# Performance work log

Hardware: AMD Instinct MI355X
Metric: run time of the kernel (lower is better)

## Reference

```python
import jax, jax.numpy as jnp
import numpy as np

K = 3          # kernel size
PAD = 1        # (K-1)//2, stride=1, dilation=1


def _modulated_deform_conv(depth, offset, mask, w, b):
    """torchvision deform_conv2d with in_ch=out_ch=1, stride=1, pad=1, dil=1.
    depth:  [B,1,H,W]
    offset: [B,2*K*K,H,W]  interleaved (dy, dx) per kernel tap
    mask:   [B,K*K,H,W]    modulation scalars
    w:      [1,1,K,K]      conv weights (ones buffer)
    b:      [1]            bias (zeros buffer)
    """
    B, _, H, W = depth.shape
    kk = K * K
    img = depth[:, 0]                                    # [B,H,W]

    off = offset.reshape(B, kk, 2, H, W)
    dy, dx = off[:, :, 0], off[:, :, 1]                  # [B,kk,H,W]

    # integer tap offsets of the 3x3 kernel
    ky, kx = jnp.meshgrid(jnp.arange(K), jnp.arange(K), indexing='ij')
    ky = ky.reshape(kk).astype(depth.dtype)
    kx = kx.reshape(kk).astype(depth.dtype)

    iy = jnp.arange(H, dtype=depth.dtype)
    ix = jnp.arange(W, dtype=depth.dtype)
    # sampling coords per output pixel per tap: [B,kk,H,W]
    y = iy[None, None, :, None] - PAD + ky[None, :, None, None] + dy
    x = ix[None, None, None, :] - PAD + kx[None, :, None, None] + dx

    y0f = jnp.floor(y); x0f = jnp.floor(x)
    wy = y - y0f; wx = x - x0f                           # frac parts
    y0 = y0f.astype(jnp.int32); x0 = x0f.astype(jnp.int32)
    y1 = y0 + 1;  x1 = x0 + 1

    bidx = jnp.arange(B)[:, None, None, None]

    def corner(yc, xc):
        inb = (yc >= 0) & (yc < H) & (xc >= 0) & (xc < W)
        v = img[bidx, jnp.clip(yc, 0, H - 1), jnp.clip(xc, 0, W - 1)]
        return jnp.where(inb, v, jnp.zeros((), depth.dtype))

    sampled = (corner(y0, x0) * (1 - wy) * (1 - wx)
             + corner(y0, x1) * (1 - wy) * wx
             + corner(y1, x0) * wy * (1 - wx)
             + corner(y1, x1) * wy * wx)                 # [B,kk,H,W]

    wk = w.reshape(1, kk, 1, 1)
    out = jnp.sum(sampled * mask * wk, axis=1) + b[0]    # [B,H,W]
    return out[:, None]                                  # [B,1,H,W]


def setup_inputs() -> dict:
    key = jax.random.key(0)
    k1, k2, k3 = jax.random.split(key, 3)
    B, H, W = 8, 512, 512
    depth  = jax.random.normal(k1, (B, 1, H, W), dtype=jnp.float32)
    weight = jax.random.uniform(k2, (B, K * K, H, W), dtype=jnp.float32)
    offset = jax.random.normal(k3, (B, 2 * K * K, H, W), dtype=jnp.float32)
    w = jnp.ones((1, 1, K, K), dtype=jnp.float32)   # buffer 'w'
    b = jnp.zeros((1,), dtype=jnp.float32)          # buffer 'b'
    return {"depth": depth, "weight": weight, "offset": offset, "w": w, "b": b}


def reference(depth, weight, offset, w, b):
    return _modulated_deform_conv(depth, offset, weight, w, b)
```

## Files before the change

### kernel.cpp

```cpp
#include <hip/hip_runtime.h>


#define KK 9
#define PAD 1
#define H 512
#define W 512
#define HW (H * W)

#define TX 64
#define TY 16
#define HALO 8
#define LW (TX + 2 * HALO)
#define LH (TY + 2 * HALO)

typedef float f2 __attribute__((ext_vector_type(2)));

__device__ __forceinline__ float bilin_global(const float* __restrict__ img,
                                              float y, float x) {
    float y0f = floorf(y);
    float x0f = floorf(x);
    int y0 = (int)y0f;
    int x0 = (int)x0f;
    float wy = y - y0f;
    float wx = x - x0f;
    int y1 = y0 + 1;
    int x1 = x0 + 1;

    bool y0i = (y0 >= 0) & (y0 < H);
    bool y1i = (y1 >= 0) & (y1 < H);
    bool x0i = (x0 >= 0) & (x0 < W);
    bool x1i = (x1 >= 0) & (x1 < W);

    int y0c = min(max(y0, 0), H - 1);
    int y1c = min(max(y1, 0), H - 1);
    int x0c = min(max(x0, 0), W - 1);
    int x1c = min(max(x1, 0), W - 1);

    float v00 = (y0i & x0i) ? img[y0c * W + x0c] : 0.0f;
    float v01 = (y0i & x1i) ? img[y0c * W + x1c] : 0.0f;
    float v10 = (y1i & x0i) ? img[y1c * W + x0c] : 0.0f;
    float v11 = (y1i & x1i) ? img[y1c * W + x1c] : 0.0f;

    float omwy = 1.0f - wy;
    float omwx = 1.0f - wx;
    return fmaf(v00 * omwy, omwx,
           fmaf(v01 * omwy, wx,
           fmaf(v10 * wy,   omwx, v11 * wy * wx)));
}

__device__ __forceinline__ float sample_tile(const float* __restrict__ S,
                                             const float* __restrict__ img,
                                             int tY0, int tX0,
                                             float sy, float sx) {
    const float y0f = floorf(sy);
    const float x0f = floorf(sx);
    const float wy = sy - y0f;
    const float wx = sx - x0f;
    const int ly0 = (int)y0f - tY0;
    const int lx0 = (int)x0f - tX0;

    if (((unsigned)ly0 < (unsigned)(LH - 1)) &
        ((unsigned)lx0 < (unsigned)(LW - 1))) {
        const int s = ly0 * LW + lx0;
        const float v00 = S[s];
        const float v01 = S[s + 1];
        const float v10 = S[s + LW];
        const float v11 = S[s + LW + 1];
        const float omwy = 1.0f - wy;
        const float omwx = 1.0f - wx;
        return fmaf(v00 * omwy, omwx,
               fmaf(v01 * omwy, wx,
               fmaf(v10 * wy,   omwx, v11 * wy * wx)));
    }
    return bilin_global(img, sy, sx);
}

__global__ __launch_bounds__(256, 4) void dcn_kernel(
    const float* __restrict__ depth,
    const float* __restrict__ mask,
    const float* __restrict__ offset,
    const float* __restrict__ w9,
    const float* __restrict__ bias,
    float* __restrict__ out) {
    __shared__ float S[LH * LW];

    const int b  = blockIdx.z;
    const int bx = blockIdx.x;
    const int by = blockIdx.y;
    const int tX0 = bx * TX - HALO;
    const int tY0 = by * TY - HALO;

    const float* __restrict__ img = depth + (long)b * HW;

    for (int i = threadIdx.x; i < LH * LW; i += 256) {
        const int ly = i / LW;
        const int lx = i - ly * LW;
        const int gy = tY0 + ly;
        const int gx = tX0 + lx;
        float v = 0.0f;
        if (((unsigned)gy < (unsigned)H) & ((unsigned)gx < (unsigned)W))
            v = img[gy * W + gx];
        S[i] = v;
    }
    __syncthreads();

    const int xp = threadIdx.x & 31;
    const int yr = threadIdx.x >> 5;
    const int tx  = bx * TX + 2 * xp;
    const int ty0 = by * TY + yr;
    const int ty1 = ty0 + 8;

    const float* __restrict__ msk = mask   + ((long)b * KK)     * HW;
    const float* __restrict__ off = offset + ((long)b * 2 * KK) * HW;

    const float bs = bias[0];
    float a00 = bs, a01 = bs, a10 = bs, a11 = bs;

    const int pix0 = ty0 * W + tx;
    const int pix1 = ty1 * W + tx;

    #pragma unroll 3
    for (int k = 0; k < KK; ++k) {
        const int ky = k / 3;
        const int kx = k - ky * 3;
        const float wk = w9[k];
        const float syb0 = (float)(ty0 - PAD + ky);
        const float syb1 = (float)(ty1 - PAD + ky);
        const float sxb  = (float)(tx  - PAD + kx);

        const f2 dy0 = *(const f2*)(off + (2 * k) * HW + pix0);
        const f2 dx0 = *(const f2*)(off + (2 * k + 1) * HW + pix0);
        const f2 m0  = *(const f2*)(msk + k * HW + pix0);
        const f2 dy1 = *(const f2*)(off + (2 * k) * HW + pix1);
        const f2 dx1 = *(const f2*)(off + (2 * k + 1) * HW + pix1);
        const f2 m1  = *(const f2*)(msk + k * HW + pix1);

        a00 = fmaf(sample_tile(S, img, tY0, tX0, syb0 + dy0.x, sxb + 0.0f + dx0.x),
                   m0.x * wk, a00);
        a01 = fmaf(sample_tile(S, img, tY0, tX0, syb0 + dy0.y, sxb + 1.0f + dx0.y),
                   m0.y * wk, a01);
        a10 = fmaf(sample_tile(S, img, tY0, tX0, syb1 + dy1.x, sxb + 0.0f + dx1.x),
                   m1.x * wk, a10);
        a11 = fmaf(sample_tile(S, img, tY0, tX0, syb1 + dy1.y, sxb + 1.0f + dx1.y),
                   m1.y * wk, a11);
    }

    float* __restrict__ o = out + (long)b * HW;
    f2 r0; r0.x = a00; r0.y = a01;
    f2 r1; r1.x = a10; r1.y = a11;
    *(f2*)(o + pix0) = r0;
    *(f2*)(o + pix1) = r1;
}

extern "C" void kernel_launch(void* const* d_in, const int* in_sizes, int n_in,
                              void* d_out, int out_size, void* d_ws, size_t ws_size,
                              hipStream_t stream) {
    const float* depth  = (const float*)d_in[0];
    const float* mask   = (const float*)d_in[1];
    const float* offset = (const float*)d_in[2];
    const float* w9     = (const float*)d_in[3];
    const float* bias   = (const float*)d_in[4];
    float* out = (float*)d_out;

    const int B = in_sizes[0] / HW;

    dim3 block(256);
    dim3 grid(W / TX, H / TY, B);
    dcn_kernel<<<grid, block, 0, stream>>>(depth, mask, offset, w9, bias, out);
}
```

Measured before the change: 279.4 us.

## Halve tile height and prefetch all offset/mask loads up front

```diff
diff --git a/kernel.cpp b/kernel.cpp
--- a/kernel.cpp
+++ b/kernel.cpp
@@ -8,7 +8,7 @@
 #define HW (H * W)
 
 #define TX 64
-#define TY 16
+#define TY 8
 #define HALO 8
 #define LW (TX + 2 * HALO)
 #define LH (TY + 2 * HALO)
@@ -75,7 +75,7 @@
     return bilin_global(img, sy, sx);
 }
 
-__global__ __launch_bounds__(256, 4) void dcn_kernel(
+__global__ void dcn_kernel(
     const float* __restrict__ depth,
     const float* __restrict__ mask,
     const float* __restrict__ offset,
@@ -106,50 +106,42 @@
 
     const int xp = threadIdx.x & 31;
     const int yr = threadIdx.x >> 5;
-    const int tx  = bx * TX + 2 * xp;
-    const int ty0 = by * TY + yr;
-    const int ty1 = ty0 + 8;
+    const int tx = bx * TX + 2 * xp;
+    const int ty = by * TY + yr;
+    const int pix = ty * W + tx;
 
-    const float* __restrict__ msk = mask   + ((long)b * KK)     * HW;
-    const float* __restrict__ off = offset + ((long)b * 2 * KK) * HW;
+    const float* __restrict__ msk = mask   + ((long)b * KK)     * HW + pix;
+    const float* __restrict__ off = offset + ((long)b * 2 * KK) * HW + pix;
+
+    f2 dyv[KK], dxv[KK], mv[KK];
+    #pragma unroll
+    for (int k = 0; k < KK; ++k) {
+        dyv[k] = *(const f2*)(off + (2 * k) * HW);
+        dxv[k] = *(const f2*)(off + (2 * k + 1) * HW);
+        mv[k]  = *(const f2*)(msk + k * HW);
+    }
 
     const float bs = bias[0];
-    float a00 = bs, a01 = bs, a10 = bs, a11 = bs;
+    float a0 = bs, a1 = bs;
+    const float syb = (float)(ty - PAD);
+    const float sxb = (float)(tx - PAD);
 
-    const int pix0 = ty0 * W + tx;
-    const int pix1 = ty1 * W + tx;
-
-    #pragma unroll 3
+    #pragma unroll
     for (int k = 0; k < KK; ++k) {
         const int ky = k / 3;
         const int kx = k - ky * 3;
         const float wk = w9[k];
-        const float syb0 = (float)(ty0 - PAD + ky);
-        const float syb1 = (float)(ty1 - PAD + ky);
-        const float sxb  = (float)(tx  - PAD + kx);
+        const float sy = syb + (float)ky;
+        const float sx = sxb + (float)kx;
 
-        const f2 dy0 = *(const f2*)(off + (2 * k) * HW + pix0);
-        const f2 dx0 = *(const f2*)(off + (2 * k + 1) * HW + pix0);
-        const f2 m0  = *(const f2*)(msk + k * HW + pix0);
-        const f2 dy1 = *(const f2*)(off + (2 * k) * HW + pix1);
-        const f2 dx1 = *(const f2*)(off + (2 * k + 1) * HW + pix1);
-        const f2 m1  = *(const f2*)(msk + k * HW + pix1);
-
-        a00 = fmaf(sample_tile(S, img, tY0, tX0, syb0 + dy0.x, sxb + 0.0f + dx0.x),
-                   m0.x * wk, a00);
-        a01 = fmaf(sample_tile(S, img, tY0, tX0, syb0 + dy0.y, sxb + 1.0f + dx0.y),
-                   m0.y * wk, a01);
-        a10 = fmaf(sample_tile(S, img, tY0, tX0, syb1 + dy1.x, sxb + 0.0f + dx1.x),
-                   m1.x * wk, a10);
-        a11 = fmaf(sample_tile(S, img, tY0, tX0, syb1 + dy1.y, sxb + 1.0f + dx1.y),
-                   m1.y * wk, a11);
+        a0 = fmaf(sample_tile(S, img, tY0, tX0, sy + dyv[k].x, sx + 0.0f + dxv[k].x),
+                  mv[k].x * wk, a0);
+        a1 = fmaf(sample_tile(S, img, tY0, tX0, sy + dyv[k].y, sx + 1.0f + dxv[k].y),
+                  mv[k].y * wk, a1);
     }
 
-    float* __restrict__ o = out + (long)b * HW;
-    f2 r0; r0.x = a00; r0.y = a01;
-    f2 r1; r1.x = a10; r1.y = a11;
-    *(f2*)(o + pix0) = r0;
-    *(f2*)(o + pix1) = r1;
+    f2 r; r.x = a0; r.y = a1;
+    *(f2*)(out + (long)b * HW + pix) = r;
 }
 
 extern "C" void kernel_launch(void* const* d_in, const int* in_sizes, int n_in,
```

New measurement: 277.0 us. About the same (-0.8%).
